# Optimization experiments

Hardware: AMD Instinct MI355X
Metric: run time of the kernel (lower is better)

## Reference

```python
import jax, jax.numpy as jnp
import numpy as np

B, N, E = 8, 100000, 300000
_CLIP = 1.0 - 1e-7  # tiny margin inside [-1,1] for numerically safe arccos


def setup_inputs() -> dict:
    key = jax.random.key(0)
    k1, k2, k3 = jax.random.split(key, 3)
    vert1 = jax.random.normal(k1, (B, N, 3), dtype=jnp.float32)
    vert2 = jax.random.normal(k2, (B, N, 3), dtype=jnp.float32)
    edge_points = jax.random.randint(k3, (B, E, 4), 0, N, dtype=jnp.int64)
    return {"vert1": vert1, "vert2": vert2, "edge_points": edge_points}


def _dihedral_angle(verts, ep):
    # verts: (N,3), ep: (E,4) = [v0, v1, opp_a, opp_b]
    def face_normal(side):
        # MeshCNN-style indexing: side in {0, 3}
        i = side // 2
        p0 = verts[ep[:, i]]                      # (E,3)
        ea = verts[ep[:, i + 2]] - p0             # edge to opposite vertex
        eb = verts[ep[:, 1 - i]] - p0             # shared edge
        n = jnp.cross(ea, eb)
        return n / jnp.clip(jnp.linalg.norm(n, axis=-1, keepdims=True), 1e-12)

    na = face_normal(0)
    nb = face_normal(3)
    dot = jnp.clip(jnp.sum(na * nb, axis=-1), -_CLIP, _CLIP)
    return jnp.pi - jnp.arccos(dot)              # (E,)


def reference(vert1, vert2, edge_points):
    angles1 = jax.vmap(_dihedral_angle)(vert1, edge_points)  # (B,E)
    angles2 = jax.vmap(_dihedral_angle)(vert2, edge_points)  # (B,E)
    per_batch = jnp.mean((angles1 - angles2) ** 2, axis=-1)  # MSE metric per mesh -> (B,)
    return jnp.mean(per_batch)                               # reduction='mean'
```

## Files before the change

### kernel.cpp

```cpp
#include <hip/hip_runtime.h>

#define NB 8
#define NV 100000
#define NE 300000
#define CLIPV 0.9999999f

#define TPB 256
#define EPT 2
#define EPB (TPB * EPT)
#define CHUNKS ((NE + EPB - 1) / EPB)

typedef int v4i __attribute__((ext_vector_type(4)));

struct F3 { float x, y, z; };

__device__ __forceinline__ F3 loadv(const float* __restrict__ v, int i) {
    const float* p = v + 3LL * i;
    F3 r; r.x = p[0]; r.y = p[1]; r.z = p[2]; return r;
}
__device__ __forceinline__ F3 sub3(F3 a, F3 b) {
    F3 r; r.x = a.x - b.x; r.y = a.y - b.y; r.z = a.z - b.z; return r;
}
__device__ __forceinline__ F3 cross3(F3 a, F3 b) {
    F3 r;
    r.x = a.y * b.z - a.z * b.y;
    r.y = a.z * b.x - a.x * b.z;
    r.z = a.x * b.y - a.y * b.x;
    return r;
}

__device__ __forceinline__ float edge_angle(F3 p0, F3 p1, F3 p2, F3 p3) {
    F3 na = cross3(sub3(p2, p0), sub3(p1, p0));
    F3 nb = cross3(sub3(p3, p1), sub3(p0, p1));
    float la = fmaxf(sqrtf(na.x * na.x + na.y * na.y + na.z * na.z), 1e-12f);
    float lb = fmaxf(sqrtf(nb.x * nb.x + nb.y * nb.y + nb.z * nb.z), 1e-12f);
    float d = (na.x * nb.x + na.y * nb.y + na.z * nb.z) * (1.0f / la) * (1.0f / lb);
    d = fminf(fmaxf(d, -CLIPV), CLIPV);
    return 3.14159265358979323846f - acosf(d);
}

__global__ void mdal_zero_ws_kernel(double* __restrict__ ws) {
    if (threadIdx.x == 0 && blockIdx.x == 0) ws[0] = 0.0;
}

__global__ __launch_bounds__(TPB, 4) void mdal_main_kernel(
    const float* __restrict__ vert1,
    const float* __restrict__ vert2,
    const int* __restrict__ edge_points,
    double* __restrict__ ws)
{
    const int bid = blockIdx.x;
    const int b = bid & (NB - 1);
    const int chunk = bid >> 3;

    const v4i* __restrict__ ep =
        reinterpret_cast<const v4i*>(edge_points) + (long long)b * NE;
    const float* __restrict__ v1 = vert1 + (long long)b * NV * 3;
    const float* __restrict__ v2 = vert2 + (long long)b * NV * 3;

    const int e0 = chunk * EPB + threadIdx.x;

    v4i idx[EPT];
    bool ok[EPT];
    #pragma unroll
    for (int k = 0; k < EPT; ++k) {
        const int e = e0 + k * TPB;
        ok[k] = (e < NE);
        if (ok[k]) {
            idx[k] = __builtin_nontemporal_load(&ep[e]);
        } else {
            idx[k] = (v4i){0, 0, 0, 0};
        }
    }

    F3 A[EPT][4], Bv[EPT][4];
    #pragma unroll
    for (int k = 0; k < EPT; ++k) {
        A[k][0] = loadv(v1, idx[k].x);
        A[k][1] = loadv(v1, idx[k].y);
        A[k][2] = loadv(v1, idx[k].z);
        A[k][3] = loadv(v1, idx[k].w);
        Bv[k][0] = loadv(v2, idx[k].x);
        Bv[k][1] = loadv(v2, idx[k].y);
        Bv[k][2] = loadv(v2, idx[k].z);
        Bv[k][3] = loadv(v2, idx[k].w);
    }

    double acc = 0.0;
    #pragma unroll
    for (int k = 0; k < EPT; ++k) {
        float a1 = edge_angle(A[k][0], A[k][1], A[k][2], A[k][3]);
        float a2 = edge_angle(Bv[k][0], Bv[k][1], Bv[k][2], Bv[k][3]);
        float d = a1 - a2;
        if (ok[k]) acc += (double)d * (double)d;
    }

    for (int off = 32; off > 0; off >>= 1)
        acc += __shfl_down(acc, off);

    __shared__ double sdata[TPB / 64];
    const int lane = threadIdx.x & 63;
    const int wave = threadIdx.x >> 6;
    if (lane == 0) sdata[wave] = acc;
    __syncthreads();
    if (threadIdx.x == 0) {
        double s = 0.0;
        #pragma unroll
        for (int w = 0; w < TPB / 64; ++w) s += sdata[w];
        atomicAdd(ws, s);
    }
}

__global__ void mdal_finalize_kernel(const double* __restrict__ ws,
                                     float* __restrict__ out) {
    if (threadIdx.x == 0 && blockIdx.x == 0)
        out[0] = (float)(ws[0] / (double)((long long)NB * NE));
}

extern "C" void kernel_launch(void* const* d_in, const int* in_sizes, int n_in,
                              void* d_out, int out_size, void* d_ws, size_t ws_size,
                              hipStream_t stream) {
    const float* vert1 = (const float*)d_in[0];
    const float* vert2 = (const float*)d_in[1];
    const int* edge_points = (const int*)d_in[2];
    float* out = (float*)d_out;
    double* ws = (double*)d_ws;

    mdal_zero_ws_kernel<<<1, 64, 0, stream>>>(ws);

    mdal_main_kernel<<<CHUNKS * NB, TPB, 0, stream>>>(vert1, vert2, edge_points, ws);

    mdal_finalize_kernel<<<1, 64, 0, stream>>>(ws, out);
}
```

Baseline: 180.8 us.

## Repack vert1/vert2 into interleaved 32-byte records for vectorized gathers

Adds a pre-pass kernel that interleaves the two vertex arrays into one 8-float record per vertex in the workspace. The main kernel then gathers each vertex of both meshes with two 16-byte loads instead of six scalar loads from two separate arrays, cutting the number of gather transactions and cache lines touched. In exchange it adds an extra kernel launch and a full read/write pass over the vertex data every call. It falls back to the old path if the workspace is too small.

Result: faster. 163.8 us (-9.4%).

```diff
diff --git a/kernel.cpp b/kernel.cpp
--- a/kernel.cpp
+++ b/kernel.cpp
@@ -9,8 +9,13 @@
 #define EPT 2
 #define EPB (TPB * EPT)
 #define CHUNKS ((NE + EPB - 1) / EPB)
+#define VCHUNKS ((NV + TPB - 1) / TPB)
+
+#define PK_OFF 256
+#define PK_BYTES ((size_t)NB * NV * 8 * sizeof(float))
 
 typedef int v4i __attribute__((ext_vector_type(4)));
+typedef float v4f __attribute__((ext_vector_type(4)));
 
 struct F3 { float x, y, z; };
 
@@ -41,6 +46,100 @@
 
 __global__ void mdal_zero_ws_kernel(double* __restrict__ ws) {
     if (threadIdx.x == 0 && blockIdx.x == 0) ws[0] = 0.0;
+}
+
+__global__ __launch_bounds__(TPB) void mdal_repack_kernel(
+    const float* __restrict__ vert1,
+    const float* __restrict__ vert2,
+    float* __restrict__ pk)
+{
+    const int bid = blockIdx.x;
+    const int b = bid & (NB - 1);
+    const int chunk = bid >> 3;
+    const int v = chunk * TPB + threadIdx.x;
+    if (v >= NV) return;
+    const long long src = ((long long)b * NV + v) * 3;
+    const long long dst = ((long long)b * NV + v) * 8;
+    float x1 = vert1[src], y1 = vert1[src + 1], z1 = vert1[src + 2];
+    float x2 = vert2[src], y2 = vert2[src + 1], z2 = vert2[src + 2];
+    v4f lo = {x1, y1, z1, x2};
+    v4f hi = {y2, z2, 0.0f, 0.0f};
+    *reinterpret_cast<v4f*>(pk + dst) = lo;
+    *reinterpret_cast<v4f*>(pk + dst + 4) = hi;
+}
+
+__global__ __launch_bounds__(TPB, 4) void mdal_main_pk_kernel(
+    const float* __restrict__ pk,
+    const int* __restrict__ edge_points,
+    double* __restrict__ ws)
+{
+    const int bid = blockIdx.x;
+    const int b = bid & (NB - 1);
+    const int chunk = bid >> 3;
+
+    const v4i* __restrict__ ep =
+        reinterpret_cast<const v4i*>(edge_points) + (long long)b * NE;
+    const float* __restrict__ pkb = pk + (long long)b * NV * 8;
+
+    const int e0 = chunk * EPB + threadIdx.x;
+
+    v4i idx[EPT];
+    bool ok[EPT];
+    #pragma unroll
+    for (int k = 0; k < EPT; ++k) {
+        const int e = e0 + k * TPB;
+        ok[k] = (e < NE);
+        if (ok[k]) {
+            idx[k] = __builtin_nontemporal_load(&ep[e]);
+        } else {
+            idx[k] = (v4i){0, 0, 0, 0};
+        }
+    }
+
+    v4f L[EPT][4], H[EPT][4];
+    #pragma unroll
+    for (int k = 0; k < EPT; ++k) {
+        #pragma unroll
+        for (int j = 0; j < 4; ++j) {
+            const int vid = (j == 0) ? idx[k].x : (j == 1) ? idx[k].y
+                          : (j == 2) ? idx[k].z : idx[k].w;
+            const v4f* p = reinterpret_cast<const v4f*>(pkb + (long long)vid * 8);
+            L[k][j] = p[0];
+            H[k][j] = p[1];
+        }
+    }
+
+    __builtin_amdgcn_sched_barrier(0);
+
+    double acc = 0.0;
+    #pragma unroll
+    for (int k = 0; k < EPT; ++k) {
+        F3 A[4], Bv[4];
+        #pragma unroll
+        for (int j = 0; j < 4; ++j) {
+            A[j].x = L[k][j].x; A[j].y = L[k][j].y; A[j].z = L[k][j].z;
+            Bv[j].x = L[k][j].w; Bv[j].y = H[k][j].x; Bv[j].z = H[k][j].y;
+        }
+        float a1 = edge_angle(A[0], A[1], A[2], A[3]);
+        float a2 = edge_angle(Bv[0], Bv[1], Bv[2], Bv[3]);
+        float d = a1 - a2;
+        if (ok[k]) acc += (double)d * (double)d;
+    }
+
+    for (int off = 32; off > 0; off >>= 1)
+        acc += __shfl_down(acc, off);
+
+    __shared__ double sdata[TPB / 64];
+    const int lane = threadIdx.x & 63;
+    const int wave = threadIdx.x >> 6;
+    if (lane == 0) sdata[wave] = acc;
+    __syncthreads();
+    if (threadIdx.x == 0) {
+        double s = 0.0;
+        #pragma unroll
+        for (int w = 0; w < TPB / 64; ++w) s += sdata[w];
+        atomicAdd(ws, s);
+    }
 }
 
 __global__ __launch_bounds__(TPB, 4) void mdal_main_kernel(
@@ -128,7 +227,13 @@
 
     mdal_zero_ws_kernel<<<1, 64, 0, stream>>>(ws);
 
-    mdal_main_kernel<<<CHUNKS * NB, TPB, 0, stream>>>(vert1, vert2, edge_points, ws);
+    if (ws_size >= PK_OFF + PK_BYTES) {
+        float* pk = (float*)((char*)d_ws + PK_OFF);
+        mdal_repack_kernel<<<VCHUNKS * NB, TPB, 0, stream>>>(vert1, vert2, pk);
+        mdal_main_pk_kernel<<<CHUNKS * NB, TPB, 0, stream>>>(pk, edge_points, ws);
+    } else {
+        mdal_main_kernel<<<CHUNKS * NB, TPB, 0, stream>>>(vert1, vert2, edge_points, ws);
+    }
 
     mdal_finalize_kernel<<<1, 64, 0, stream>>>(ws, out);
 }
```
